# Optimization experiments

Measured on AMD Instinct MI355X. Metric: run time of the kernel, lower is better.

## Reference

```python
import jax, jax.numpy as jnp
import numpy as np

N, E, F_IN, H, C, G, NC = 50000, 800000, 128, 4, 64, 512, 10
NEG_SLOPE = 0.2


def setup_inputs() -> dict:
    key = jax.random.key(0)
    ks = jax.random.split(key, 16)
    s = lambda fan: 1.0 / np.sqrt(fan)
    inp = {
        'x': jax.random.normal(ks[0], (N, F_IN), jnp.float32),
        'edge_index': jax.random.randint(ks[1], (2, E), 0, N, jnp.int64),
        'batch': jnp.sort(jax.random.randint(ks[2], (N,), 0, G, jnp.int64)),
        # conv1: F_IN -> H*C, concat
        'W1': jax.random.normal(ks[3], (F_IN, H * C), jnp.float32) * s(F_IN),
        'a_src1': jax.random.normal(ks[4], (H, C), jnp.float32) * s(C),
        'a_dst1': jax.random.normal(ks[5], (H, C), jnp.float32) * s(C),
        'b1': jnp.zeros((H * C,), jnp.float32),
        # conv2: H*C -> H*C, concat
        'W2': jax.random.normal(ks[6], (H * C, H * C), jnp.float32) * s(H * C),
        'a_src2': jax.random.normal(ks[7], (H, C), jnp.float32) * s(C),
        'a_dst2': jax.random.normal(ks[8], (H, C), jnp.float32) * s(C),
        'b2': jnp.zeros((H * C,), jnp.float32),
        # conv3: H*C -> C, concat=False (mean over heads)
        'W3': jax.random.normal(ks[9], (H * C, H * C), jnp.float32) * s(H * C),
        'a_src3': jax.random.normal(ks[10], (H, C), jnp.float32) * s(C),
        'a_dst3': jax.random.normal(ks[11], (H, C), jnp.float32) * s(C),
        'b3': jnp.zeros((C,), jnp.float32),
        # final linear: C -> NC
        'Wl': jax.random.normal(ks[12], (C, NC), jnp.float32) * s(C),
        'bl': jnp.zeros((NC,), jnp.float32),
    }
    return inp


def _gat_conv(x, src, dst, W, a_src, a_dst, b, concat):
    n = x.shape[0]
    h = (x @ W).reshape(n, H, C)                       # [N,H,C]
    al_src = jnp.sum(h * a_src, axis=-1)               # [N,H]
    al_dst = jnp.sum(h * a_dst, axis=-1)               # [N,H]
    e = al_src[src] + al_dst[dst]                      # [E',H] per-edge logits
    e = jax.nn.leaky_relu(e, NEG_SLOPE)
    # segment softmax over incoming edges of each dst node
    m = jax.ops.segment_max(e, dst, num_segments=n)
    ex = jnp.exp(e - m[dst])
    z = jax.ops.segment_sum(ex, dst, num_segments=n)
    alpha = ex / (z[dst] + 1e-16)                      # [E',H]
    msg = h[src] * alpha[:, :, None]                   # [E',H,C]
    out = jax.ops.segment_sum(msg, dst, num_segments=n)  # [N,H,C]
    out = out.reshape(n, H * C) if concat else out.mean(axis=1)
    return out + b


def reference(x, edge_index, batch, W1, a_src1, a_dst1, b1, W2, a_src2, a_dst2, b2,
              W3, a_src3, a_dst3, b3, Wl, bl):
    n = x.shape[0]
    loops = jnp.arange(n, dtype=edge_index.dtype)
    src = jnp.concatenate([edge_index[0], loops])      # add self-loops (PyG default)
    dst = jnp.concatenate([edge_index[1], loops])
    h = jax.nn.relu(_gat_conv(x, src, dst, W1, a_src1, a_dst1, b1, True))
    h = jax.nn.relu(_gat_conv(h, src, dst, W2, a_src2, a_dst2, b2, True))
    h = jax.nn.relu(_gat_conv(h, src, dst, W3, a_src3, a_dst3, b3, False))
    # global mean pool over graphs
    sums = jax.ops.segment_sum(h, batch, num_segments=G)          # [G,C]
    cnts = jax.ops.segment_sum(jnp.ones((n,), h.dtype), batch, num_segments=G)
    pooled = sums / jnp.maximum(cnts, 1.0)[:, None]
    # dropout is identity in eval mode
    return pooled @ Wl + bl                                       # [G,NC]
```

## Files before the change

### kernel.cpp

```cpp
#include <hip/hip_runtime.h>

#define N_NODES 50000
#define E_EDGES 800000
#define E_TOT   (E_EDGES + N_NODES)
#define F_INDIM 128
#define NHEAD   4
#define CDIM    64
#define HC      256
#define NGRAPH  512
#define NCLS    10
#define NEG_SLOPE 0.2f

typedef __attribute__((ext_vector_type(8))) _Float16 f16x8;
typedef __attribute__((ext_vector_type(8))) unsigned short ushort8;
typedef __attribute__((ext_vector_type(4))) float f32x4;

__device__ inline float leakyf(float x) { return x > 0.f ? x : NEG_SLOPE * x; }
__device__ inline unsigned short f2h(float x) {
  _Float16 h = (_Float16)x;
  return __builtin_bit_cast(unsigned short, h);
}
__device__ inline float h2f(unsigned short u) {
  return (float)__builtin_bit_cast(_Float16, u);
}

__global__ __launch_bounds__(256) void k_init_deg(int* __restrict__ deg) {
  int i = blockIdx.x * 256 + threadIdx.x;
  if (i < N_NODES) deg[i] = 1;
}

__global__ __launch_bounds__(256) void k_hist(const int* __restrict__ ei, int* __restrict__ deg) {
  int e = blockIdx.x * 256 + threadIdx.x;
  if (e < E_EDGES) atomicAdd(&deg[ei[E_EDGES + e]], 1);
}

__global__ __launch_bounds__(256) void k_scan1(const int* __restrict__ deg, int* __restrict__ incl,
                                               int* __restrict__ blksum) {
  __shared__ int s[256];
  int tid = threadIdx.x;
  int i = blockIdx.x * 256 + tid;
  int v = (i < N_NODES) ? deg[i] : 0;
  s[tid] = v;
  __syncthreads();
  for (int d = 1; d < 256; d <<= 1) {
    int t = (tid >= d) ? s[tid - d] : 0;
    __syncthreads();
    s[tid] += t;
    __syncthreads();
  }
  if (i < N_NODES) incl[i] = s[tid];
  if (tid == 255) blksum[blockIdx.x] = s[255];
}

__global__ __launch_bounds__(256) void k_scan2(int* __restrict__ blksum, int nblk) {
  __shared__ int s[256];
  int tid = threadIdx.x;
  int v = (tid < nblk) ? blksum[tid] : 0;
  s[tid] = v;
  __syncthreads();
  for (int d = 1; d < 256; d <<= 1) {
    int t = (tid >= d) ? s[tid - d] : 0;
    __syncthreads();
    s[tid] += t;
    __syncthreads();
  }
  if (tid < nblk) blksum[tid] = s[tid] - v;
}

__global__ __launch_bounds__(256) void k_scan3(const int* __restrict__ deg, int* __restrict__ off,
                                               const int* __restrict__ blksum, int* __restrict__ cursor) {
  int i = blockIdx.x * 256 + threadIdx.x;
  if (i < N_NODES) {
    int excl = off[i] - deg[i] + blksum[blockIdx.x];
    off[i] = excl;
    cursor[i] = excl;
  }
  if (i == 0) off[N_NODES] = E_TOT;
}

__global__ __launch_bounds__(256) void k_fill(const int* __restrict__ ei, int* __restrict__ cursor,
                                              int* __restrict__ csr_src) {
  int idx = blockIdx.x * 256 + threadIdx.x;
  if (idx >= E_TOT) return;
  int s, d;
  if (idx < E_EDGES) { s = ei[idx]; d = ei[E_EDGES + idx]; }
  else               { s = idx - E_EDGES; d = s; }
  int pos = atomicAdd(&cursor[d], 1);
  csr_src[pos] = s;
}

__global__ __launch_bounds__(256) void k_cvt_x(const float* __restrict__ x, unsigned short* __restrict__ xh) {
  int i = blockIdx.x * 256 + threadIdx.x;
  float4 v0 = *(const float4*)&x[(size_t)i * 8];
  float4 v1 = *(const float4*)&x[(size_t)i * 8 + 4];
  ushort8 o;
  o[0] = f2h(v0.x); o[1] = f2h(v0.y); o[2] = f2h(v0.z); o[3] = f2h(v0.w);
  o[4] = f2h(v1.x); o[5] = f2h(v1.y); o[6] = f2h(v1.z); o[7] = f2h(v1.w);
  *(ushort8*)&xh[(size_t)i * 8] = o;
}

__global__ __launch_bounds__(256) void k_cvt_wt(const float* __restrict__ W, unsigned short* __restrict__ Wt,
                                                int K) {
  int i = blockIdx.x * 256 + threadIdx.x;
  if (i < K * HC) {
    int k = i >> 8, n = i & 255;
    Wt[n * K + k] = f2h(W[i]);
  }
}

template<int K>
__global__ __launch_bounds__(256) void k_gemm_f16(const unsigned short* __restrict__ A,
                                                  const unsigned short* __restrict__ Bt,
                                                  unsigned short* __restrict__ C) {
  __shared__ unsigned short As[128 * 64];
  __shared__ unsigned short Bs[128 * 64];
  int tid = threadIdx.x;
  int w = tid >> 6, l = tid & 63;
  int wm = w >> 1, wn = w & 1;
  int m0 = blockIdx.x * 128, n0 = blockIdx.y * 128;
  f32x4 acc[4][4] = {};

  int sr = w * 32 + (l >> 3);
  int g8 = l & 7;
  int slot = g8 ^ (sr & 7);
  int fl = l & 15;

  for (int k0 = 0; k0 < K; k0 += 64) {
    uint4 va[4], vb[4];
#pragma unroll
    for (int j = 0; j < 4; ++j) {
      int ar = m0 + sr + j * 8;
      va[j] = (ar < N_NODES) ? *(const uint4*)&A[(size_t)ar * K + k0 + g8 * 8]
                             : make_uint4(0u, 0u, 0u, 0u);
      vb[j] = *(const uint4*)&Bt[(size_t)(n0 + sr + j * 8) * K + k0 + g8 * 8];
    }
    __syncthreads();
#pragma unroll
    for (int j = 0; j < 4; ++j) {
      *(uint4*)&As[(sr + j * 8) * 64 + slot * 8] = va[j];
      *(uint4*)&Bs[(sr + j * 8) * 64 + slot * 8] = vb[j];
    }
    __syncthreads();
#pragma unroll
    for (int kk = 0; kk < 2; ++kk) {
      int sl = ((kk * 4 + (l >> 4)) ^ (l & 7)) * 8;
      f16x8 af[4], bfr[4];
#pragma unroll
      for (int f = 0; f < 4; ++f) {
        af[f]  = *(const f16x8*)&As[(wm * 64 + f * 16 + fl) * 64 + sl];
        bfr[f] = *(const f16x8*)&Bs[(wn * 64 + f * 16 + fl) * 64 + sl];
      }
#pragma unroll
      for (int f = 0; f < 4; ++f)
#pragma unroll
        for (int g = 0; g < 4; ++g)
          acc[f][g] = __builtin_amdgcn_mfma_f32_16x16x32_f16(af[f], bfr[g], acc[f][g], 0, 0, 0);
    }
  }
  int cr = (l >> 4) * 4;
#pragma unroll
  for (int f = 0; f < 4; ++f) {
    int mrow = m0 + wm * 64 + f * 16 + cr;
#pragma unroll
    for (int r = 0; r < 4; ++r) {
      if (mrow + r < N_NODES) {
#pragma unroll
        for (int g = 0; g < 4; ++g)
          C[(size_t)(mrow + r) * HC + n0 + wn * 64 + g * 16 + fl] = f2h(acc[f][g][r]);
      }
    }
  }
}

__global__ __launch_bounds__(256) void k_attn(const unsigned short* __restrict__ h,
                                              const float* __restrict__ a_src, const float* __restrict__ a_dst,
                                              float* __restrict__ al_s, float* __restrict__ al_d) {
  int tid = threadIdx.x;
  int lane = tid & 63;
  int n = blockIdx.x * 8 + (tid >> 6) * 2 + (lane >> 5);
  int cg8 = (lane & 31) << 3;
  ushort8 hv = *(const ushort8*)&h[(size_t)n * HC + cg8];
  float4 s0 = *(const float4*)&a_src[cg8], s1 = *(const float4*)&a_src[cg8 + 4];
  float4 d0 = *(const float4*)&a_dst[cg8], d1 = *(const float4*)&a_dst[cg8 + 4];
  float hr[8];
#pragma unroll
  for (int i = 0; i < 8; ++i) hr[i] = h2f(hv[i]);
  float ps = hr[0] * s0.x + hr[1] * s0.y + hr[2] * s0.z + hr[3] * s0.w
           + hr[4] * s1.x + hr[5] * s1.y + hr[6] * s1.z + hr[7] * s1.w;
  float pd = hr[0] * d0.x + hr[1] * d0.y + hr[2] * d0.z + hr[3] * d0.w
           + hr[4] * d1.x + hr[5] * d1.y + hr[6] * d1.z + hr[7] * d1.w;
#pragma unroll
  for (int o = 1; o < 8; o <<= 1) { ps += __shfl_xor(ps, o); pd += __shfl_xor(pd, o); }
  if ((lane & 7) == 0) {
    int head = (lane & 31) >> 3;
    al_s[n * 4 + head] = ps;
    al_d[n * 4 + head] = pd;
  }
}

template<bool CONCAT>
__global__ __launch_bounds__(256) void k_aggregate(
    const unsigned short* __restrict__ h, const int* __restrict__ off, const int* __restrict__ csr_src,
    const float* __restrict__ al_s, const float* __restrict__ al_d,
    const float* __restrict__ bias, unsigned short* __restrict__ out_h, float* __restrict__ out_f) {
  __shared__ float s_alpha[4][64][4];
  __shared__ int   s_src[4][64];
  int tid = threadIdx.x;
  int wv = tid >> 6;
  int lane = tid & 63;
  int half_id = lane >> 5;
  int c8 = lane & 31;
  int cg8 = c8 << 3;
  int head = c8 >> 3;
  int d = blockIdx.x * 4 + wv;

  int lo  = off[d];
  int deg = off[d + 1] - lo;

  float4 adv = *(const float4*)&al_d[(size_t)d * 4];

  float m0 = -1e30f, m1 = -1e30f, m2 = -1e30f, m3 = -1e30f;
  int s0 = 0;
  float e00 = -1e30f, e01 = -1e30f, e02 = -1e30f, e03 = -1e30f;
  for (int e = lane; e < deg; e += 64) {
    int s = csr_src[lo + e];
    float4 asv = *(const float4*)&al_s[(size_t)s * 4];
    float v0 = leakyf(asv.x + adv.x);
    float v1 = leakyf(asv.y + adv.y);
    float v2 = leakyf(asv.z + adv.z);
    float v3 = leakyf(asv.w + adv.w);
    if (e == lane) { s0 = s; e00 = v0; e01 = v1; e02 = v2; e03 = v3; }
    m0 = fmaxf(m0, v0); m1 = fmaxf(m1, v1); m2 = fmaxf(m2, v2); m3 = fmaxf(m3, v3);
  }
#pragma unroll
  for (int o = 1; o < 64; o <<= 1) {
    m0 = fmaxf(m0, __shfl_xor(m0, o));
    m1 = fmaxf(m1, __shfl_xor(m1, o));
    m2 = fmaxf(m2, __shfl_xor(m2, o));
    m3 = fmaxf(m3, __shfl_xor(m3, o));
  }
  float p00 = 0.f, p01 = 0.f, p02 = 0.f, p03 = 0.f;
  if (lane < deg) {
    p00 = __expf(e00 - m0); p01 = __expf(e01 - m1);
    p02 = __expf(e02 - m2); p03 = __expf(e03 - m3);
  }
  float z0 = p00, z1 = p01, z2 = p02, z3 = p03;
  for (int e = lane + 64; e < deg; e += 64) {
    int s = csr_src[lo + e];
    float4 asv = *(const float4*)&al_s[(size_t)s * 4];
    z0 += __expf(leakyf(asv.x + adv.x) - m0);
    z1 += __expf(leakyf(asv.y + adv.y) - m1);
    z2 += __expf(leakyf(asv.z + adv.z) - m2);
    z3 += __expf(leakyf(asv.w + adv.w) - m3);
  }
#pragma unroll
  for (int o = 1; o < 64; o <<= 1) {
    z0 += __shfl_xor(z0, o); z1 += __shfl_xor(z1, o);
    z2 += __shfl_xor(z2, o); z3 += __shfl_xor(z3, o);
  }
  float zi0 = 1.f / (z0 + 1e-16f), zi1 = 1.f / (z1 + 1e-16f);
  float zi2 = 1.f / (z2 + 1e-16f), zi3 = 1.f / (z3 + 1e-16f);

  s_alpha[wv][lane][0] = p00 * zi0;
  s_alpha[wv][lane][1] = p01 * zi1;
  s_alpha[wv][lane][2] = p02 * zi2;
  s_alpha[wv][lane][3] = p03 * zi3;
  s_src[wv][lane] = s0;
  __syncthreads();

  int dcap = min(deg, 64);
  float acc[8] = {};
  int e = half_id;
  for (; e + 6 < dcap; e += 8) {
    int sv[4]; float av[4]; ushort8 hv[4];
#pragma unroll
    for (int q = 0; q < 4; ++q) {
      int ee = e + q * 2;
      sv[q] = s_src[wv][ee];
      av[q] = s_alpha[wv][ee][head];
    }
#pragma unroll
    for (int q = 0; q < 4; ++q) hv[q] = *(const ushort8*)&h[(size_t)sv[q] * HC + cg8];
#pragma unroll
    for (int q = 0; q < 4; ++q)
#pragma unroll
      for (int i = 0; i < 8; ++i) acc[i] = fmaf(av[q], h2f(hv[q][i]), acc[i]);
  }
  for (; e < dcap; e += 2) {
    int s = s_src[wv][e];
    float a = s_alpha[wv][e][head];
    ushort8 hv = *(const ushort8*)&h[(size_t)s * HC + cg8];
#pragma unroll
    for (int i = 0; i < 8; ++i) acc[i] = fmaf(a, h2f(hv[i]), acc[i]);
  }
  if (deg > 64) {
    for (int e2 = 64 + half_id; e2 < deg; e2 += 2) {
      int s = csr_src[lo + e2];
      float4 asv = *(const float4*)&al_s[(size_t)s * 4];
      float q0 = __expf(leakyf(asv.x + adv.x) - m0) * zi0;
      float q1 = __expf(leakyf(asv.y + adv.y) - m1) * zi1;
      float q2 = __expf(leakyf(asv.z + adv.z) - m2) * zi2;
      float q3 = __expf(leakyf(asv.w + adv.w) - m3) * zi3;
      float a = head == 0 ? q0 : (head == 1 ? q1 : (head == 2 ? q2 : q3));
      ushort8 hv = *(const ushort8*)&h[(size_t)s * HC + cg8];
#pragma unroll
      for (int i = 0; i < 8; ++i) acc[i] = fmaf(a, h2f(hv[i]), acc[i]);
    }
  }

#pragma unroll
  for (int i = 0; i < 8; ++i) acc[i] += __shfl_xor(acc[i], 32);

  if (CONCAT) {
    if (lane < 32) {
      float4 b0 = *(const float4*)&bias[cg8];
      float4 b1v = *(const float4*)&bias[cg8 + 4];
      ushort8 o;
      o[0] = f2h(fmaxf(acc[0] + b0.x, 0.f));
      o[1] = f2h(fmaxf(acc[1] + b0.y, 0.f));
      o[2] = f2h(fmaxf(acc[2] + b0.z, 0.f));
      o[3] = f2h(fmaxf(acc[3] + b0.w, 0.f));
      o[4] = f2h(fmaxf(acc[4] + b1v.x, 0.f));
      o[5] = f2h(fmaxf(acc[5] + b1v.y, 0.f));
      o[6] = f2h(fmaxf(acc[6] + b1v.z, 0.f));
      o[7] = f2h(fmaxf(acc[7] + b1v.w, 0.f));
      *(ushort8*)&out_h[(size_t)d * HC + cg8] = o;
    }
  } else {
#pragma unroll
    for (int i = 0; i < 8; ++i) {
      acc[i] += __shfl_xor(acc[i], 8);
      acc[i] += __shfl_xor(acc[i], 16);
    }
    if (lane < 8) {
      int c0 = lane << 3;
      float4 bb0 = *(const float4*)&bias[c0];
      float4 bb1 = *(const float4*)&bias[c0 + 4];
      float4 v0, v1;
      v0.x = fmaxf(acc[0] * 0.25f + bb0.x, 0.f);
      v0.y = fmaxf(acc[1] * 0.25f + bb0.y, 0.f);
      v0.z = fmaxf(acc[2] * 0.25f + bb0.z, 0.f);
      v0.w = fmaxf(acc[3] * 0.25f + bb0.w, 0.f);
      v1.x = fmaxf(acc[4] * 0.25f + bb1.x, 0.f);
      v1.y = fmaxf(acc[5] * 0.25f + bb1.y, 0.f);
      v1.z = fmaxf(acc[6] * 0.25f + bb1.z, 0.f);
      v1.w = fmaxf(acc[7] * 0.25f + bb1.w, 0.f);
      *(float4*)&out_f[(size_t)d * CDIM + c0] = v0;
      *(float4*)&out_f[(size_t)d * CDIM + c0 + 4] = v1;
    }
  }
}

__device__ inline int lower_bound_i(const int* __restrict__ a, int n, int key) {
  int lo = 0, hi = n;
  while (lo < hi) { int mid = (lo + hi) >> 1; if (a[mid] < key) lo = mid + 1; else hi = mid; }
  return lo;
}

__global__ __launch_bounds__(256) void k_pool(const float* __restrict__ x, const int* __restrict__ batch,
                                              const float* __restrict__ Wl, const float* __restrict__ bl,
                                              float* __restrict__ out) {
  int g = blockIdx.x, tid = threadIdx.x;
  int lo = lower_bound_i(batch, N_NODES, g);
  int hi = lower_bound_i(batch, N_NODES, g + 1);
  int c = tid & 63, sl = tid >> 6;
  float acc = 0.f;
  for (int n = lo + sl; n < hi; n += 4)
    acc += x[(size_t)n * CDIM + c];
  __shared__ float s[256];
  __shared__ float pooled[64];
  s[tid] = acc;
  __syncthreads();
  if (tid < 64) {
    float cnt = fmaxf((float)(hi - lo), 1.f);
    pooled[tid] = (s[tid] + s[tid + 64] + s[tid + 128] + s[tid + 192]) / cnt;
  }
  __syncthreads();
  if (tid < NCLS) {
    float o = bl[tid];
    for (int cc = 0; cc < CDIM; ++cc)
      o = fmaf(pooled[cc], Wl[cc * NCLS + tid], o);
    out[g * NCLS + tid] = o;
  }
}

extern "C" void kernel_launch(void* const* d_in, const int* in_sizes, int n_in,
                              void* d_out, int out_size, void* d_ws, size_t ws_size,
                              hipStream_t stream) {
  const float* x     = (const float*)d_in[0];
  const int*   ei    = (const int*)d_in[1];
  const int*   batch = (const int*)d_in[2];
  const float* W1  = (const float*)d_in[3];
  const float* as1 = (const float*)d_in[4];
  const float* ad1 = (const float*)d_in[5];
  const float* b1  = (const float*)d_in[6];
  const float* W2  = (const float*)d_in[7];
  const float* as2 = (const float*)d_in[8];
  const float* ad2 = (const float*)d_in[9];
  const float* b2  = (const float*)d_in[10];
  const float* W3  = (const float*)d_in[11];
  const float* as3 = (const float*)d_in[12];
  const float* ad3 = (const float*)d_in[13];
  const float* b3  = (const float*)d_in[14];
  const float* Wl  = (const float*)d_in[15];
  const float* bl  = (const float*)d_in[16];
  float* out = (float*)d_out;

  char* ws = (char*)d_ws;
  size_t o = 0;
  auto alloc = [&](size_t bytes) -> void* {
    void* p = ws + o;
    o += (bytes + 255) & ~(size_t)255;
    return p;
  };
  unsigned short* hbuf  = (unsigned short*)alloc((size_t)N_NODES * HC * 2);
  unsigned short* abuf  = (unsigned short*)alloc((size_t)N_NODES * HC * 2);
  float*          bufC  = (float*)alloc((size_t)N_NODES * CDIM * 4);
  unsigned short* x_h   = (unsigned short*)alloc((size_t)N_NODES * F_INDIM * 2);
  unsigned short* Wt1   = (unsigned short*)alloc((size_t)HC * F_INDIM * 2);
  unsigned short* Wt2   = (unsigned short*)alloc((size_t)HC * HC * 2);
  unsigned short* Wt3   = (unsigned short*)alloc((size_t)HC * HC * 2);
  float* al_s  = (float*)alloc((size_t)N_NODES * 4 * 4);
  float* al_d  = (float*)alloc((size_t)N_NODES * 4 * 4);
  int*   deg   = (int*)alloc((size_t)N_NODES * 4);
  int*   off   = (int*)alloc((size_t)(N_NODES + 1) * 4);
  int*   cursor= (int*)alloc((size_t)N_NODES * 4);
  int*   blksum= (int*)alloc(1024);
  int*   csr   = (int*)alloc((size_t)E_TOT * 4);

  int nblk = (N_NODES + 255) / 256;
  k_init_deg<<<nblk, 256, 0, stream>>>(deg);
  k_hist<<<(E_EDGES + 255) / 256, 256, 0, stream>>>(ei, deg);
  k_scan1<<<nblk, 256, 0, stream>>>(deg, off, blksum);
  k_scan2<<<1, 256, 0, stream>>>(blksum, nblk);
  k_scan3<<<nblk, 256, 0, stream>>>(deg, off, blksum, cursor);
  k_fill<<<(E_TOT + 255) / 256, 256, 0, stream>>>(ei, cursor, csr);

  k_cvt_x<<<(N_NODES * F_INDIM / 8 + 255) / 256, 256, 0, stream>>>(x, x_h);
  k_cvt_wt<<<(F_INDIM * HC + 255) / 256, 256, 0, stream>>>(W1, Wt1, F_INDIM);
  k_cvt_wt<<<(HC * HC + 255) / 256, 256, 0, stream>>>(W2, Wt2, HC);
  k_cvt_wt<<<(HC * HC + 255) / 256, 256, 0, stream>>>(W3, Wt3, HC);

  dim3 ggrid((N_NODES + 127) / 128, HC / 128);
  int nagg = N_NODES / 4;
  int natt = N_NODES / 8;
  k_gemm_f16<F_INDIM><<<ggrid, 256, 0, stream>>>(x_h, Wt1, hbuf);
  k_attn<<<natt, 256, 0, stream>>>(hbuf, as1, ad1, al_s, al_d);
  k_aggregate<true><<<nagg, 256, 0, stream>>>(hbuf, off, csr, al_s, al_d, b1, abuf, nullptr);
  k_gemm_f16<HC><<<ggrid, 256, 0, stream>>>(abuf, Wt2, hbuf);
  k_attn<<<natt, 256, 0, stream>>>(hbuf, as2, ad2, al_s, al_d);
  k_aggregate<true><<<nagg, 256, 0, stream>>>(hbuf, off, csr, al_s, al_d, b2, abuf, nullptr);
  k_gemm_f16<HC><<<ggrid, 256, 0, stream>>>(abuf, Wt3, hbuf);
  k_attn<<<natt, 256, 0, stream>>>(hbuf, as3, ad3, al_s, al_d);
  k_aggregate<false><<<nagg, 256, 0, stream>>>(hbuf, off, csr, al_s, al_d, b3, nullptr, bufC);
  k_pool<<<NGRAPH, 256, 0, stream>>>(bufC, batch, Wl, bl, out);
}
```

Measured before the change: 453.2 us.

## Fuse attention logits into GEMM epilogue and use single-pass unnormalized softmax

Computes the per-node source/destination attention logits directly from the GEMM accumulators, so the separate attention kernel and its reread of h are gone. Aggregation now uses one pass that accumulates exp(logit) without subtracting the segment max. Normalization by the sum is applied once at the end, and the block barrier and an extra edge pass are dropped. The gather loop is unrolled to 8 edges per step. Skipping the max subtraction risks exp overflow for large logits.

```diff
diff --git a/kernel.cpp b/kernel.cpp
--- a/kernel.cpp
+++ b/kernel.cpp
@@ -111,7 +111,11 @@
 template<int K>
 __global__ __launch_bounds__(256) void k_gemm_f16(const unsigned short* __restrict__ A,
                                                   const unsigned short* __restrict__ Bt,
-                                                  unsigned short* __restrict__ C) {
+                                                  unsigned short* __restrict__ C,
+                                                  const float* __restrict__ a_src,
+                                                  const float* __restrict__ a_dst,
+                                                  float* __restrict__ al_s,
+                                                  float* __restrict__ al_d) {
   __shared__ unsigned short As[128 * 64];
   __shared__ unsigned short Bs[128 * 64];
   int tid = threadIdx.x;
@@ -170,31 +174,33 @@
       }
     }
   }
-}
-
-__global__ __launch_bounds__(256) void k_attn(const unsigned short* __restrict__ h,
-                                              const float* __restrict__ a_src, const float* __restrict__ a_dst,
-                                              float* __restrict__ al_s, float* __restrict__ al_d) {
-  int tid = threadIdx.x;
-  int lane = tid & 63;
-  int n = blockIdx.x * 8 + (tid >> 6) * 2 + (lane >> 5);
-  int cg8 = (lane & 31) << 3;
-  ushort8 hv = *(const ushort8*)&h[(size_t)n * HC + cg8];
-  float4 s0 = *(const float4*)&a_src[cg8], s1 = *(const float4*)&a_src[cg8 + 4];
-  float4 d0 = *(const float4*)&a_dst[cg8], d1 = *(const float4*)&a_dst[cg8 + 4];
-  float hr[8];
-#pragma unroll
-  for (int i = 0; i < 8; ++i) hr[i] = h2f(hv[i]);
-  float ps = hr[0] * s0.x + hr[1] * s0.y + hr[2] * s0.z + hr[3] * s0.w
-           + hr[4] * s1.x + hr[5] * s1.y + hr[6] * s1.z + hr[7] * s1.w;
-  float pd = hr[0] * d0.x + hr[1] * d0.y + hr[2] * d0.z + hr[3] * d0.w
-           + hr[4] * d1.x + hr[5] * d1.y + hr[6] * d1.z + hr[7] * d1.w;
-#pragma unroll
-  for (int o = 1; o < 8; o <<= 1) { ps += __shfl_xor(ps, o); pd += __shfl_xor(pd, o); }
-  if ((lane & 7) == 0) {
-    int head = (lane & 31) >> 3;
-    al_s[n * 4 + head] = ps;
-    al_d[n * 4 + head] = pd;
+  int head = blockIdx.y * 2 + wn;
+  float as_r[4], ad_r[4];
+#pragma unroll
+  for (int g = 0; g < 4; ++g) {
+    as_r[g] = a_src[head * 64 + g * 16 + fl];
+    ad_r[g] = a_dst[head * 64 + g * 16 + fl];
+  }
+#pragma unroll
+  for (int f = 0; f < 4; ++f) {
+#pragma unroll
+    for (int r = 0; r < 4; ++r) {
+      float ps = 0.f, pd = 0.f;
+#pragma unroll
+      for (int g = 0; g < 4; ++g) {
+        ps = fmaf(as_r[g], acc[f][g][r], ps);
+        pd = fmaf(ad_r[g], acc[f][g][r], pd);
+      }
+#pragma unroll
+      for (int o = 1; o < 16; o <<= 1) { ps += __shfl_xor(ps, o); pd += __shfl_xor(pd, o); }
+      if (fl == 0) {
+        int row = m0 + wm * 64 + f * 16 + cr + r;
+        if (row < N_NODES) {
+          al_s[row * 4 + head] = ps;
+          al_d[row * 4 + head] = pd;
+        }
+      }
+    }
   }
 }
 
@@ -203,7 +209,7 @@
     const unsigned short* __restrict__ h, const int* __restrict__ off, const int* __restrict__ csr_src,
     const float* __restrict__ al_s, const float* __restrict__ al_d,
     const float* __restrict__ bias, unsigned short* __restrict__ out_h, float* __restrict__ out_f) {
-  __shared__ float s_alpha[4][64][4];
+  __shared__ float s_p[4][64][4];
   __shared__ int   s_src[4][64];
   int tid = threadIdx.x;
   int wv = tid >> 6;
@@ -219,39 +225,20 @@
 
   float4 adv = *(const float4*)&al_d[(size_t)d * 4];
 
-  float m0 = -1e30f, m1 = -1e30f, m2 = -1e30f, m3 = -1e30f;
-  int s0 = 0;
-  float e00 = -1e30f, e01 = -1e30f, e02 = -1e30f, e03 = -1e30f;
+  float z0 = 0.f, z1 = 0.f, z2 = 0.f, z3 = 0.f;
   for (int e = lane; e < deg; e += 64) {
     int s = csr_src[lo + e];
     float4 asv = *(const float4*)&al_s[(size_t)s * 4];
-    float v0 = leakyf(asv.x + adv.x);
-    float v1 = leakyf(asv.y + adv.y);
-    float v2 = leakyf(asv.z + adv.z);
-    float v3 = leakyf(asv.w + adv.w);
-    if (e == lane) { s0 = s; e00 = v0; e01 = v1; e02 = v2; e03 = v3; }
-    m0 = fmaxf(m0, v0); m1 = fmaxf(m1, v1); m2 = fmaxf(m2, v2); m3 = fmaxf(m3, v3);
-  }
-#pragma unroll
-  for (int o = 1; o < 64; o <<= 1) {
-    m0 = fmaxf(m0, __shfl_xor(m0, o));
-    m1 = fmaxf(m1, __shfl_xor(m1, o));
-    m2 = fmaxf(m2, __shfl_xor(m2, o));
-    m3 = fmaxf(m3, __shfl_xor(m3, o));
-  }
-  float p00 = 0.f, p01 = 0.f, p02 = 0.f, p03 = 0.f;
-  if (lane < deg) {
-    p00 = __expf(e00 - m0); p01 = __expf(e01 - m1);
-    p02 = __expf(e02 - m2); p03 = __expf(e03 - m3);
-  }
-  float z0 = p00, z1 = p01, z2 = p02, z3 = p03;
-  for (int e = lane + 64; e < deg; e += 64) {
-    int s = csr_src[lo + e];
-    float4 asv = *(const float4*)&al_s[(size_t)s * 4];
-    z0 += __expf(leakyf(asv.x + adv.x) - m0);
-    z1 += __expf(leakyf(asv.y + adv.y) - m1);
-    z2 += __expf(leakyf(asv.z + adv.z) - m2);
-    z3 += __expf(leakyf(asv.w + adv.w) - m3);
+    float p0 = __expf(leakyf(asv.x + adv.x));
+    float p1 = __expf(leakyf(asv.y + adv.y));
+    float p2 = __expf(leakyf(asv.z + adv.z));
+    float p3 = __expf(leakyf(asv.w + adv.w));
+    if (e < 64) {
+      s_p[wv][e][0] = p0; s_p[wv][e][1] = p1;
+      s_p[wv][e][2] = p2; s_p[wv][e][3] = p3;
+      s_src[wv][e] = s;
+    }
+    z0 += p0; z1 += p1; z2 += p2; z3 += p3;
   }
 #pragma unroll
   for (int o = 1; o < 64; o <<= 1) {
@@ -260,56 +247,53 @@
   }
   float zi0 = 1.f / (z0 + 1e-16f), zi1 = 1.f / (z1 + 1e-16f);
   float zi2 = 1.f / (z2 + 1e-16f), zi3 = 1.f / (z3 + 1e-16f);
-
-  s_alpha[wv][lane][0] = p00 * zi0;
-  s_alpha[wv][lane][1] = p01 * zi1;
-  s_alpha[wv][lane][2] = p02 * zi2;
-  s_alpha[wv][lane][3] = p03 * zi3;
-  s_src[wv][lane] = s0;
-  __syncthreads();
+  float zih = head == 0 ? zi0 : (head == 1 ? zi1 : (head == 2 ? zi2 : zi3));
 
   int dcap = min(deg, 64);
   float acc[8] = {};
   int e = half_id;
-  for (; e + 6 < dcap; e += 8) {
-    int sv[4]; float av[4]; ushort8 hv[4];
-#pragma unroll
-    for (int q = 0; q < 4; ++q) {
+  for (; e + 14 < dcap; e += 16) {
+    int sv[8]; float pv[8]; ushort8 hv[8];
+#pragma unroll
+    for (int q = 0; q < 8; ++q) {
       int ee = e + q * 2;
       sv[q] = s_src[wv][ee];
-      av[q] = s_alpha[wv][ee][head];
-    }
-#pragma unroll
-    for (int q = 0; q < 4; ++q) hv[q] = *(const ushort8*)&h[(size_t)sv[q] * HC + cg8];
-#pragma unroll
-    for (int q = 0; q < 4; ++q)
-#pragma unroll
-      for (int i = 0; i < 8; ++i) acc[i] = fmaf(av[q], h2f(hv[q][i]), acc[i]);
+      pv[q] = s_p[wv][ee][head];
+    }
+#pragma unroll
+    for (int q = 0; q < 8; ++q) hv[q] = *(const ushort8*)&h[(size_t)sv[q] * HC + cg8];
+#pragma unroll
+    for (int q = 0; q < 8; ++q)
+#pragma unroll
+      for (int i = 0; i < 8; ++i) acc[i] = fmaf(pv[q], h2f(hv[q][i]), acc[i]);
   }
   for (; e < dcap; e += 2) {
     int s = s_src[wv][e];
-    float a = s_alpha[wv][e][head];
+    float p = s_p[wv][e][head];
     ushort8 hv = *(const ushort8*)&h[(size_t)s * HC + cg8];
 #pragma unroll
-    for (int i = 0; i < 8; ++i) acc[i] = fmaf(a, h2f(hv[i]), acc[i]);
+    for (int i = 0; i < 8; ++i) acc[i] = fmaf(p, h2f(hv[i]), acc[i]);
   }
   if (deg > 64) {
     for (int e2 = 64 + half_id; e2 < deg; e2 += 2) {
       int s = csr_src[lo + e2];
       float4 asv = *(const float4*)&al_s[(size_t)s * 4];
-      float q0 = __expf(leakyf(asv.x + adv.x) - m0) * zi0;
-      float q1 = __expf(leakyf(asv.y + adv.y) - m1) * zi1;
-      float q2 = __expf(leakyf(asv.z + adv.z) - m2) * zi2;
-      float q3 = __expf(leakyf(asv.w + adv.w) - m3) * zi3;
-      float a = head == 0 ? q0 : (head == 1 ? q1 : (head == 2 ? q2 : q3));
+      float q0 = __expf(leakyf(asv.x + adv.x));
+      float q1 = __expf(leakyf(asv.y + adv.y));
+      float q2 = __expf(leakyf(asv.z + adv.z));
+      float q3 = __expf(leakyf(asv.w + adv.w));
+      float p = head == 0 ? q0 : (head == 1 ? q1 : (head == 2 ? q2 : q3));
       ushort8 hv = *(const ushort8*)&h[(size_t)s * HC + cg8];
 #pragma unroll
-      for (int i = 0; i < 8; ++i) acc[i] = fmaf(a, h2f(hv[i]), acc[i]);
-    }
-  }
-
-#pragma unroll
-  for (int i = 0; i < 8; ++i) acc[i] += __shfl_xor(acc[i], 32);
+      for (int i = 0; i < 8; ++i) acc[i] = fmaf(p, h2f(hv[i]), acc[i]);
+    }
+  }
+
+#pragma unroll
+  for (int i = 0; i < 8; ++i) {
+    acc[i] *= zih;
+    acc[i] += __shfl_xor(acc[i], 32);
+  }
 
   if (CONCAT) {
     if (lane < 32) {
@@ -443,15 +427,11 @@
 
   dim3 ggrid((N_NODES + 127) / 128, HC / 128);
   int nagg = N_NODES / 4;
-  int natt = N_NODES / 8;
-  k_gemm_f16<F_INDIM><<<ggrid, 256, 0, stream>>>(x_h, Wt1, hbuf);
-  k_attn<<<natt, 256, 0, stream>>>(hbuf, as1, ad1, al_s, al_d);
+  k_gemm_f16<F_INDIM><<<ggrid, 256, 0, stream>>>(x_h, Wt1, hbuf, as1, ad1, al_s, al_d);
   k_aggregate<true><<<nagg, 256, 0, stream>>>(hbuf, off, csr, al_s, al_d, b1, abuf, nullptr);
-  k_gemm_f16<HC><<<ggrid, 256, 0, stream>>>(abuf, Wt2, hbuf);
-  k_attn<<<natt, 256, 0, stream>>>(hbuf, as2, ad2, al_s, al_d);
+  k_gemm_f16<HC><<<ggrid, 256, 0, stream>>>(abuf, Wt2, hbuf, as2, ad2, al_s, al_d);
   k_aggregate<true><<<nagg, 256, 0, stream>>>(hbuf, off, csr, al_s, al_d, b2, abuf, nullptr);
-  k_gemm_f16<HC><<<ggrid, 256, 0, stream>>>(abuf, Wt3, hbuf);
-  k_attn<<<natt, 256, 0, stream>>>(hbuf, as3, ad3, al_s, al_d);
+  k_gemm_f16<HC><<<ggrid, 256, 0, stream>>>(abuf, Wt3, hbuf, as3, ad3, al_s, al_d);
   k_aggregate<false><<<nagg, 256, 0, stream>>>(hbuf, off, csr, al_s, al_d, b3, nullptr, bufC);
   k_pool<<<NGRAPH, 256, 0, stream>>>(bufC, batch, Wl, bl, out);
 }
```

New measurement: 454.3 us. About the same (+0.2%).
